# Performance work log

Measured on AMD Instinct MI355X. Metric: run time of the kernel, lower is better.

Reference implementation:

```python
import jax, jax.numpy as jnp
import numpy as np

N, MAX_NB, H, L, V, B, M = 16384, 15, 512, 128, 1024, 256, 65536


def setup_inputs() -> dict:
    key = jax.random.key(0)
    ks = jax.random.split(key, 32)
    s = 0.02  # param init scale
    inp = {
        'x_ids': jax.random.randint(ks[0], (N,), 0, V, dtype=jnp.int32),
        'contexts': jax.random.randint(ks[1], (N,), 0, B, dtype=jnp.int32),
        'nei_idx': jax.random.randint(ks[2], (N, MAX_NB), 0, M, dtype=jnp.int32),
        'nei_mask': jax.random.randint(ks[3], (N, MAX_NB), 0, 2, dtype=jnp.int32),
        'o_idx': jax.random.randint(ks[4], (N, MAX_NB), 0, M, dtype=jnp.int32),
        'o_mask': jax.random.randint(ks[5], (N, MAX_NB), 0, 2, dtype=jnp.int32),
        'H_msg': jax.random.normal(ks[6], (M, H), jnp.float32),
        'x_tree_vecs': jax.random.normal(ks[7], (B, L), jnp.float32),
        'embedding': jax.random.normal(ks[8], (V, H), jnp.float32) * s,
        'Wz_w': jax.random.normal(ks[9], (H, 2 * H), jnp.float32) * s,
        'Wz_b': jnp.zeros((H,), jnp.float32),
        'Wr_w': jax.random.normal(ks[10], (H, H), jnp.float32) * s,
        'Wr_b': jnp.zeros((H,), jnp.float32),
        'Ur_w': jax.random.normal(ks[11], (H, H), jnp.float32) * s,
        'Wh_w': jax.random.normal(ks[12], (H, 2 * H), jnp.float32) * s,
        'Wh_b': jnp.zeros((H,), jnp.float32),
        'W_w': jax.random.normal(ks[13], (H, H + L), jnp.float32) * s,
        'W_b': jnp.zeros((H,), jnp.float32),
        'Wo_w': jax.random.normal(ks[14], (V, H), jnp.float32) * s,
        'Wo_b': jnp.zeros((V,), jnp.float32),
        'Ui_w': jax.random.normal(ks[15], (H, 2 * H), jnp.float32) * s,
        'Ui_b': jnp.zeros((H,), jnp.float32),
        'U_w': jax.random.normal(ks[16], (H, H + L), jnp.float32) * s,
        'U_b': jnp.zeros((H,), jnp.float32),
        'Uo_w': jax.random.normal(ks[17], (1, H), jnp.float32) * s,
        'Uo_b': jnp.zeros((1,), jnp.float32),
    }
    return inp


def _gru(x, h_nei, Wz_w, Wz_b, Wr_w, Wr_b, Ur_w, Wh_w, Wh_b):
    # x: [N,H], h_nei: [N,MAX_NB,H]
    sum_h = h_nei.sum(axis=1)
    z = jax.nn.sigmoid(jnp.concatenate([x, sum_h], axis=1) @ Wz_w.T + Wz_b)
    r1 = (x @ Wr_w.T + Wr_b)[:, None, :]          # [N,1,H]
    r2 = jnp.einsum('nkh,gh->nkg', h_nei, Ur_w)   # U_r(h_nei), no bias
    r = jax.nn.sigmoid(r1 + r2)
    sum_gated = (r * h_nei).sum(axis=1)
    pre_h = jnp.tanh(jnp.concatenate([x, sum_gated], axis=1) @ Wh_w.T + Wh_b)
    return (1.0 - z) * sum_h + z * pre_h


def reference(x_ids, contexts, nei_idx, nei_mask, o_idx, o_mask, H_msg,
              x_tree_vecs, embedding, Wz_w, Wz_b, Wr_w, Wr_b, Ur_w,
              Wh_w, Wh_b, W_w, W_b, Wo_w, Wo_b, Ui_w, Ui_b, U_w, U_b,
              Uo_w, Uo_b):
    x = embedding[x_ids]                                   # [N,H]
    h_nei = H_msg[nei_idx] * nei_mask[..., None].astype(H_msg.dtype)  # [N,NB,H]
    o_nei = H_msg[o_idx] * o_mask[..., None].astype(H_msg.dtype)
    new_h = _gru(x, h_nei, Wz_w, Wz_b, Wr_w, Wr_b, Ur_w, Wh_w, Wh_b)
    cur_o = o_nei.sum(axis=1)                              # [N,H]
    ctx = x_tree_vecs[contexts]                            # [N,L]
    # word prediction: aggregate(new_h, contexts, x_tree_vecs, 'word')
    w_hid = jax.nn.relu(jnp.concatenate([new_h, ctx], axis=1) @ W_w.T + W_b)
    word_scores = w_hid @ Wo_w.T + Wo_b                    # [N,V]
    # stop prediction: U_i(cat(x, cur_o)) -> aggregate(..., 'stop')
    stop_h = jax.nn.relu(jnp.concatenate([x, cur_o], axis=1) @ Ui_w.T + Ui_b)
    s_hid = jax.nn.relu(jnp.concatenate([stop_h, ctx], axis=1) @ U_w.T + U_b)
    stop_scores = s_hid @ Uo_w.T + Uo_b                    # [N,1]
    return jnp.concatenate([word_scores, stop_scores], axis=1)  # [N,V+1]
```

## Files before the change

### kernel.cpp

```cpp
#include <hip/hip_runtime.h>
#include <hip/hip_bf16.h>

typedef unsigned short u16;
typedef unsigned int u32;
typedef __attribute__((ext_vector_type(8))) short s8v;
typedef __attribute__((ext_vector_type(4))) float f4v;

#define HDIM 512
#define NNODE 16384
#define NB 15

__device__ __forceinline__ u16 f2bu(float x) {
  union { float f; u32 i; } v; v.f = x;
  u32 r = v.i + 0x7FFFu + ((v.i >> 16) & 1u);
  return (u16)(r >> 16);
}
__device__ __forceinline__ float bu2f(u16 u) {
  union { u32 i; float f; } v; v.i = ((u32)u) << 16;
  return v.f;
}
__device__ __forceinline__ u32 pk(float a, float b) {
  return (u32)f2bu(a) | ((u32)f2bu(b) << 16);
}
__device__ __forceinline__ float sigm(float x) {
  return __builtin_amdgcn_rcpf(1.f + __expf(-x));
}
__device__ __forceinline__ void gl16(const void* g, void* l) {
  __builtin_amdgcn_global_load_lds(
      (const __attribute__((address_space(1))) u32*)g,
      (__attribute__((address_space(3))) u32*)l, 16, 0, 0);
}

__global__ __launch_bounds__(256) void k_cvt_all(
    const float* Wz_w, const float* Wr_w, const float* Wh_w, const float* Ui_w,
    const float* Ur_w, const float* W_w, const float* U_w, const float* Wo_w,
    const float* emb, const float* xtree,
    const float* Wz_b, const float* Wr_b, const float* Wh_b, const float* Ui_b,
    const float* W_b, const float* U_b,
    u16* wcat, u16* wz_h, u16* wh_h, u16* ui_h, u16* ur, u16* w_n, u16* u_n,
    u16* ccat, u16* wo, u16* emb_bf, u16* xt_bf, float* ebias, float* cbias) {
  int seg = blockIdx.y;
  const float* src = nullptr; u16* dst = nullptr;
  const float* fsrc = nullptr; float* fdst = nullptr;
  int R = 0, Cs = 0, c0 = 0, C = 0, fn = 0;
  switch (seg) {
    case 0:  src = Wz_w; dst = wcat;              R = 512;  Cs = 1024; c0 = 0;   C = 512; break;
    case 1:  src = Wr_w; dst = wcat + 512 * 512;  R = 512;  Cs = 512;  c0 = 0;   C = 512; break;
    case 2:  src = Wh_w; dst = wcat + 1024 * 512; R = 512;  Cs = 1024; c0 = 0;   C = 512; break;
    case 3:  src = Ui_w; dst = wcat + 1536 * 512; R = 512;  Cs = 1024; c0 = 0;   C = 512; break;
    case 4:  src = Wz_w; dst = wz_h;              R = 512;  Cs = 1024; c0 = 512; C = 512; break;
    case 5:  src = Wh_w; dst = wh_h;              R = 512;  Cs = 1024; c0 = 512; C = 512; break;
    case 6:  src = Ui_w; dst = ui_h;              R = 512;  Cs = 1024; c0 = 512; C = 512; break;
    case 7:  src = Ur_w; dst = ur;                R = 512;  Cs = 512;  c0 = 0;   C = 512; break;
    case 8:  src = W_w;  dst = w_n;               R = 512;  Cs = 640;  c0 = 0;   C = 512; break;
    case 9:  src = U_w;  dst = u_n;               R = 512;  Cs = 640;  c0 = 0;   C = 512; break;
    case 10: src = W_w;  dst = ccat;              R = 512;  Cs = 640;  c0 = 512; C = 128; break;
    case 11: src = U_w;  dst = ccat + 512 * 128;  R = 512;  Cs = 640;  c0 = 512; C = 128; break;
    case 12: src = Wo_w; dst = wo;                R = 1024; Cs = 512;  c0 = 0;   C = 512; break;
    case 13: src = emb;  dst = emb_bf;            R = 1024; Cs = 512;  c0 = 0;   C = 512; break;
    case 14: src = xtree; dst = xt_bf;            R = 256;  Cs = 128;  c0 = 0;   C = 128; break;
    case 15: fsrc = Wz_b; fdst = ebias;        fn = 512; break;
    case 16: fsrc = Wr_b; fdst = ebias + 512;  fn = 512; break;
    case 17: fsrc = Wh_b; fdst = ebias + 1024; fn = 512; break;
    case 18: fsrc = Ui_b; fdst = ebias + 1536; fn = 512; break;
    case 19: fsrc = W_b;  fdst = cbias;        fn = 512; break;
    case 20: fsrc = U_b;  fdst = cbias + 512;  fn = 512; break;
  }
  int i = blockIdx.x * 256 + threadIdx.x;
  if (fdst) { if (i < fn) fdst[i] = fsrc[i]; return; }
  int e0 = i * 8;
  if (e0 >= R * C) return;
  int r = e0 / C, c = e0 - r * C;
  const float* s = src + (size_t)r * Cs + c0 + c;
  float4 a = *reinterpret_cast<const float4*>(s);
  float4 b = *reinterpret_cast<const float4*>(s + 4);
  uint4 o = {pk(a.x, a.y), pk(a.z, a.w), pk(b.x, b.y), pk(b.z, b.w)};
  *reinterpret_cast<uint4*>(&dst[e0]) = o;
}

__global__ void k_cvtH(const float* __restrict__ src, u16* __restrict__ HR) {
  size_t i = ((size_t)blockIdx.x * 256 + threadIdx.x) * 8;
  size_t m = i >> 9, c = i & 511;
  float4 a = *reinterpret_cast<const float4*>(src + i);
  float4 b = *reinterpret_cast<const float4*>(src + i + 4);
  uint4 o = {pk(a.x, a.y), pk(a.z, a.w), pk(b.x, b.y), pk(b.z, b.w)};
  *reinterpret_cast<uint4*>(&HR[m * 1024 + c]) = o;
}

struct GP {
  const u16* A; const u16* B; int K; int lda;
  const float* gadd; int ldg; const int* gidx;
  const float* bias; const u16* shb;
  float* outf; u16* outh; int ldo;
};

template<int EP>
__device__ __forceinline__ void epi(int row, int col, float v, const GP& g) {
  if constexpr (EP == 0) {
    g.outf[(size_t)row * g.ldo + col] = v + (g.bias ? g.bias[col] : 0.f);
  } else if constexpr (EP == 3) {
    float pre = v + g.gadd[(size_t)g.gidx[row] * g.ldg + col];
    g.outh[(size_t)row * g.ldo + col] = f2bu(pre > 0.f ? pre : 0.f);
  } else {
    g.outh[(size_t)row * g.ldo + col] = f2bu(v);
  }
}

template<int EP>
__device__ void gemm_core(const GP& g, u16* AsB, u16* BsB) {
  const int tid = threadIdx.x, lane = tid & 63, w = tid >> 6;
  const int wm = (w >> 2) * 64, wn = (w & 3) * 32;
  const int nx = gridDim.x;
  int orig = blockIdx.y * nx + blockIdx.x;
  int q = (nx * gridDim.y) >> 3;
  int tile = (orig & 7) * q + (orig >> 3);
  const int n0 = (tile % nx) * 128, m0 = (tile / nx) * 128;
  const int K = g.K;

  const u16* gA[2]; const u16* gB[2]; int ls[2];
#pragma unroll
  for (int i = 0; i < 2; i++) {
    int slot = tid + i * 512;
    int r = slot >> 3, c = (slot & 7) ^ (r & 7);
    gA[i] = g.A + (size_t)(m0 + r) * g.lda + c * 8;
    gB[i] = g.B + (size_t)(n0 + r) * K + c * 8;
    ls[i] = slot * 8;
  }

  f4v acc[4][2];
  f4v z4 = {0.f, 0.f, 0.f, 0.f};
#pragma unroll
  for (int a = 0; a < 4; a++) { acc[a][0] = z4; acc[a][1] = z4; }

  const int T = K >> 6;
#pragma unroll
  for (int i = 0; i < 2; i++) gl16(gA[i], AsB + ls[i]);
#pragma unroll
  for (int i = 0; i < 2; i++) gl16(gB[i], BsB + ls[i]);

  int cur = 0;
  for (int t = 0; t < T; t++) {
    __syncthreads();
    if (t + 1 < T) {
      int k0 = (t + 1) * 64;
      u16* as = AsB + (cur ^ 1) * 8192;
      u16* bs = BsB + (cur ^ 1) * 8192;
#pragma unroll
      for (int i = 0; i < 2; i++) gl16(gA[i] + k0, as + ls[i]);
#pragma unroll
      for (int i = 0; i < 2; i++) gl16(gB[i] + k0, bs + ls[i]);
    }
    const u16* as = AsB + cur * 8192;
    const u16* bs = BsB + cur * 8192;
#pragma unroll
    for (int ks = 0; ks < 2; ks++) {
      s8v af[4], bf[2];
      int cc = ks * 4 + (lane >> 4);
#pragma unroll
      for (int i = 0; i < 4; i++) {
        int R = wm + i * 16 + (lane & 15);
        af[i] = *reinterpret_cast<const s8v*>(&as[R * 64 + (cc ^ (R & 7)) * 8]);
      }
#pragma unroll
      for (int i = 0; i < 2; i++) {
        int C = wn + i * 16 + (lane & 15);
        bf[i] = *reinterpret_cast<const s8v*>(&bs[C * 64 + (cc ^ (C & 7)) * 8]);
      }
#pragma unroll
      for (int mi = 0; mi < 4; mi++)
#pragma unroll
        for (int ni = 0; ni < 2; ni++)
          acc[mi][ni] = __builtin_amdgcn_mfma_f32_16x16x32_bf16(
              af[mi], bf[ni], acc[mi][ni], 0, 0, 0);
    }
    cur ^= 1;
  }
#pragma unroll
  for (int mi = 0; mi < 4; mi++)
#pragma unroll
    for (int ni = 0; ni < 2; ni++)
#pragma unroll
      for (int r = 0; r < 4; r++) {
        int row = m0 + wm + mi * 16 + (lane >> 4) * 4 + r;
        int col = n0 + wn + ni * 16 + (lane & 15);
        epi<EP>(row, col, acc[mi][ni][r], g);
      }
}

template<int EP>
__global__ __launch_bounds__(512, 4) void k_gemm(GP g) {
  __shared__ u16 As[2 * 128 * 64], Bs[2 * 128 * 64];
  gemm_core<EP>(g, As, Bs);
}

template<int EPa, int EPb>
__global__ __launch_bounds__(512, 4) void k_pair(GP a, GP b) {
  __shared__ u16 As[2 * 128 * 64], Bs[2 * 128 * 64];
  if (blockIdx.z == 0) gemm_core<EPa>(a, As, Bs);
  else gemm_core<EPb>(b, As, Bs);
}

__global__ __launch_bounds__(512, 4) void k_zn(
    const u16* __restrict__ sumh, const u16* __restrict__ sg,
    const u16* __restrict__ Wz, const u16* __restrict__ Wh,
    const float* __restrict__ E_z, const float* __restrict__ E_h, int ldg,
    const int* __restrict__ gidx, u16* __restrict__ newh) {
  __shared__ u16 As1[128 * 64], Bs1[128 * 64], As2[128 * 64], Bs2[128 * 64];
  const int tid = threadIdx.x, lane = tid & 63, w = tid >> 6;
  const int wm = (w >> 2) * 64, wn = (w & 3) * 32;
  const int nx = gridDim.x;
  int orig = blockIdx.y * nx + blockIdx.x;
  int q = (nx * gridDim.y) >> 3;
  int tile = (orig & 7) * q + (orig >> 3);
  const int n0 = (tile % nx) * 128, m0 = (tile / nx) * 128;

  const u16 *gA1[2], *gA2[2], *gB1[2], *gB2[2]; int ls[2];
#pragma unroll
  for (int i = 0; i < 2; i++) {
    int slot = tid + i * 512;
    int r = slot >> 3, c = (slot & 7) ^ (r & 7);
    gA1[i] = sumh + (size_t)(m0 + r) * HDIM + c * 8;
    gA2[i] = sg + (size_t)(m0 + r) * HDIM + c * 8;
    gB1[i] = Wz + (size_t)(n0 + r) * HDIM + c * 8;
    gB2[i] = Wh + (size_t)(n0 + r) * HDIM + c * 8;
    ls[i] = slot * 8;
  }

  f4v az[4][2], ah[4][2];
  f4v z4 = {0.f, 0.f, 0.f, 0.f};
#pragma unroll
  for (int a = 0; a < 4; a++) {
    az[a][0] = z4; az[a][1] = z4; ah[a][0] = z4; ah[a][1] = z4;
  }

  for (int k0 = 0; k0 < HDIM; k0 += 64) {
    __syncthreads();
#pragma unroll
    for (int i = 0; i < 2; i++) gl16(gA1[i] + k0, As1 + ls[i]);
#pragma unroll
    for (int i = 0; i < 2; i++) gl16(gB1[i] + k0, Bs1 + ls[i]);
#pragma unroll
    for (int i = 0; i < 2; i++) gl16(gA2[i] + k0, As2 + ls[i]);
#pragma unroll
    for (int i = 0; i < 2; i++) gl16(gB2[i] + k0, Bs2 + ls[i]);
    __syncthreads();
#pragma unroll
    for (int ks = 0; ks < 2; ks++) {
      int cc = ks * 4 + (lane >> 4);
      {
        s8v af[4], bf[2];
#pragma unroll
        for (int i = 0; i < 4; i++) {
          int R = wm + i * 16 + (lane & 15);
          af[i] = *reinterpret_cast<const s8v*>(&As1[R * 64 + (cc ^ (R & 7)) * 8]);
        }
#pragma unroll
        for (int i = 0; i < 2; i++) {
          int C = wn + i * 16 + (lane & 15);
          bf[i] = *reinterpret_cast<const s8v*>(&Bs1[C * 64 + (cc ^ (C & 7)) * 8]);
        }
#pragma unroll
        for (int mi = 0; mi < 4; mi++)
#pragma unroll
          for (int ni = 0; ni < 2; ni++)
            az[mi][ni] = __builtin_amdgcn_mfma_f32_16x16x32_bf16(
                af[mi], bf[ni], az[mi][ni], 0, 0, 0);
      }
      {
        s8v af[4], bf[2];
#pragma unroll
        for (int i = 0; i < 4; i++) {
          int R = wm + i * 16 + (lane & 15);
          af[i] = *reinterpret_cast<const s8v*>(&As2[R * 64 + (cc ^ (R & 7)) * 8]);
        }
#pragma unroll
        for (int i = 0; i < 2; i++) {
          int C = wn + i * 16 + (lane & 15);
          bf[i] = *reinterpret_cast<const s8v*>(&Bs2[C * 64 + (cc ^ (C & 7)) * 8]);
        }
#pragma unroll
        for (int mi = 0; mi < 4; mi++)
#pragma unroll
          for (int ni = 0; ni < 2; ni++)
            ah[mi][ni] = __builtin_amdgcn_mfma_f32_16x16x32_bf16(
                af[mi], bf[ni], ah[mi][ni], 0, 0, 0);
      }
    }
  }
#pragma unroll
  for (int mi = 0; mi < 4; mi++)
#pragma unroll
    for (int r = 0; r < 4; r++) {
      int row = m0 + wm + mi * 16 + (lane >> 4) * 4 + r;
      int xid = gidx[row];
      const float* ez = E_z + (size_t)xid * ldg;
      const float* eh = E_h + (size_t)xid * ldg;
#pragma unroll
      for (int ni = 0; ni < 2; ni++) {
        int col = n0 + wn + ni * 16 + (lane & 15);
        float zv = sigm(az[mi][ni][r] + ez[col]);
        float pre = tanhf(ah[mi][ni][r] + eh[col]);
        float sh = bu2f(sumh[(size_t)row * HDIM + col]);
        newh[(size_t)row * HDIM + col] = f2bu((1.f - zv) * sh + zv * pre);
      }
    }
}

__global__ __launch_bounds__(256) void k_gsr(
    const u16* __restrict__ HR,
    const float* __restrict__ E_r, int ldg, const int* __restrict__ x_ids,
    const int* __restrict__ nei_idx, const int* __restrict__ nei_mask,
    const int* __restrict__ o_idx, const int* __restrict__ o_mask,
    u16* __restrict__ sum_h_bf, u16* __restrict__ sg_bf,
    u16* __restrict__ cur_o_bf) {
  int n = blockIdx.x;
  int t = threadIdx.x;
  __shared__ int sidx[NB], smsk[NB], soid[NB], somk[NB];
  __shared__ int sx;
  if (t < NB) {
    sidx[t] = nei_idx[(size_t)n * NB + t];
    smsk[t] = nei_mask[(size_t)n * NB + t];
  } else if (t >= 64 && t < 64 + NB) {
    int k = t - 64;
    soid[k] = o_idx[(size_t)n * NB + k];
    somk[k] = o_mask[(size_t)n * NB + k];
  } else if (t == 128) {
    sx = x_ids[n];
  }
  __syncthreads();
  int c = t * 2;
  const float2 e = *reinterpret_cast<const float2*>(E_r + (size_t)sx * ldg + c);
  float s0 = 0.f, s1 = 0.f, g0 = 0.f, g1 = 0.f, o0 = 0.f, o1 = 0.f;
#pragma unroll
  for (int k = 0; k < NB; k++) {
    if (smsk[k]) {
      const u16* row = HR + (size_t)sidx[k] * 1024;
      u32 hv = *reinterpret_cast<const u32*>(row + c);
      u32 rv = *reinterpret_cast<const u32*>(row + 512 + c);
      float h0 = bu2f((u16)hv), h1 = bu2f((u16)(hv >> 16));
      float r0 = sigm(bu2f((u16)rv) + e.x);
      float r1 = sigm(bu2f((u16)(rv >> 16)) + e.y);
      s0 += h0; s1 += h1;
      g0 += r0 * h0; g1 += r1 * h1;
    }
    if (somk[k]) {
      u32 v = *reinterpret_cast<const u32*>(HR + (size_t)soid[k] * 1024 + c);
      o0 += bu2f((u16)v); o1 += bu2f((u16)(v >> 16));
    }
  }
  size_t b = (size_t)n * HDIM + c;
  *reinterpret_cast<u32*>(&sum_h_bf[b]) = pk(s0, s1);
  *reinterpret_cast<u32*>(&sg_bf[b]) = pk(g0, g1);
  *reinterpret_cast<u32*>(&cur_o_bf[b]) = pk(o0, o1);
}

__global__ __launch_bounds__(256) void k_stop(
    const u16* __restrict__ shid, const float* __restrict__ Uo_w,
    const float* __restrict__ Uo_b, float* __restrict__ out) {
  int n = blockIdx.x * 4 + (threadIdx.x >> 6);
  int lane = threadIdx.x & 63;
  float s = 0.f;
  for (int j = lane; j < HDIM; j += 64)
    s += bu2f(shid[(size_t)n * HDIM + j]) * Uo_w[j];
#pragma unroll
  for (int off = 32; off; off >>= 1) s += __shfl_xor(s, off, 64);
  if (lane == 0) out[(size_t)n * 1025 + 1024] = s + Uo_b[0];
}

extern "C" void kernel_launch(void* const* d_in, const int* in_sizes, int n_in,
                              void* d_out, int out_size, void* d_ws, size_t ws_size,
                              hipStream_t stream) {
  const int* x_ids = (const int*)d_in[0];
  const int* contexts = (const int*)d_in[1];
  const int* nei_idx = (const int*)d_in[2];
  const int* nei_mask = (const int*)d_in[3];
  const int* o_idx = (const int*)d_in[4];
  const int* o_mask = (const int*)d_in[5];
  const float* H_msg = (const float*)d_in[6];
  const float* xtree = (const float*)d_in[7];
  const float* emb = (const float*)d_in[8];
  const float* Wz_w = (const float*)d_in[9];  const float* Wz_b = (const float*)d_in[10];
  const float* Wr_w = (const float*)d_in[11]; const float* Wr_b = (const float*)d_in[12];
  const float* Ur_w = (const float*)d_in[13];
  const float* Wh_w = (const float*)d_in[14]; const float* Wh_b = (const float*)d_in[15];
  const float* W_w  = (const float*)d_in[16]; const float* W_b  = (const float*)d_in[17];
  const float* Wo_w = (const float*)d_in[18]; const float* Wo_b = (const float*)d_in[19];
  const float* Ui_w = (const float*)d_in[20]; const float* Ui_b = (const float*)d_in[21];
  const float* U_w  = (const float*)d_in[22]; const float* U_b  = (const float*)d_in[23];
  const float* Uo_w = (const float*)d_in[24]; const float* Uo_b = (const float*)d_in[25];
  float* out = (float*)d_out;
  const int M = 65536;

  char* base = (char*)d_ws;
  size_t ofs = 0;
  auto alloc = [&](size_t bytes) -> char* {
    char* p = base + ofs;
    ofs = (ofs + bytes + 255) & ~(size_t)255;
    return p;
  };
  u16* wcat  = (u16*)alloc((size_t)2048 * 512 * 2);
  u16* wz_h  = (u16*)alloc(512 * 512 * 2);
  u16* wh_h  = (u16*)alloc(512 * 512 * 2);
  u16* ui_h  = (u16*)alloc(512 * 512 * 2);
  u16* ur    = (u16*)alloc(512 * 512 * 2);
  u16* w_n   = (u16*)alloc(512 * 512 * 2);
  u16* u_n   = (u16*)alloc(512 * 512 * 2);
  u16* ccat  = (u16*)alloc(1024 * 128 * 2);
  u16* wo    = (u16*)alloc(1024 * 512 * 2);
  u16* emb_bf = (u16*)alloc(1024 * 512 * 2);
  u16* xt_bf  = (u16*)alloc(256 * 128 * 2);
  float* ebias = (float*)alloc(2048 * 4);
  float* cbias = (float*)alloc(1024 * 4);
  float* E_cat = (float*)alloc((size_t)1024 * 2048 * 4);
  float* C_cat = (float*)alloc((size_t)256 * 1024 * 4);
  u16* HR = (u16*)alloc((size_t)M * 1024 * 2);
  u16* sum_h_bf = (u16*)alloc((size_t)NNODE * HDIM * 2);
  u16* cur_o_bf = (u16*)alloc((size_t)NNODE * HDIM * 2);
  u16* sg_bf    = (u16*)alloc((size_t)NNODE * HDIM * 2);
  u16* newh_bf  = (u16*)alloc((size_t)NNODE * HDIM * 2);
  u16* whid_bf  = (u16*)alloc((size_t)NNODE * HDIM * 2);
  u16* stoph_bf = (u16*)alloc((size_t)NNODE * HDIM * 2);
  u16* shid_bf  = (u16*)alloc((size_t)NNODE * HDIM * 2);

  k_cvt_all<<<dim3(256, 21), dim3(256), 0, stream>>>(
      Wz_w, Wr_w, Wh_w, Ui_w, Ur_w, W_w, U_w, Wo_w, emb, xtree,
      Wz_b, Wr_b, Wh_b, Ui_b, W_b, U_b,
      wcat, wz_h, wh_h, ui_h, ur, w_n, u_n, ccat, wo, emb_bf, xt_bf,
      ebias, cbias);
  k_cvtH<<<dim3(16384), dim3(256), 0, stream>>>(H_msg, HR);

  GP ge{emb_bf, wcat, 512, 512, nullptr, 0, nullptr, ebias, nullptr,
        E_cat, nullptr, 2048};
  k_gemm<0><<<dim3(16, 8), dim3(512), 0, stream>>>(ge);
  GP gc{xt_bf, ccat, 128, 128, nullptr, 0, nullptr, cbias, nullptr,
        C_cat, nullptr, 1024};
  k_gemm<0><<<dim3(8, 2), dim3(512), 0, stream>>>(gc);

  GP gr{HR, ur, 512, 1024, nullptr, 0, nullptr, nullptr, nullptr,
        nullptr, HR + 512, 1024};
  k_gemm<4><<<dim3(4, 512), dim3(512), 0, stream>>>(gr);

  k_gsr<<<dim3(NNODE), dim3(256), 0, stream>>>(
      HR, E_cat + 512, 2048, x_ids, nei_idx, nei_mask, o_idx, o_mask,
      sum_h_bf, sg_bf, cur_o_bf);

  GP gs{cur_o_bf, ui_h, 512, 512, E_cat + 1536, 2048, x_ids, nullptr, nullptr,
        nullptr, stoph_bf, 512};
  k_gemm<3><<<dim3(4, 128), dim3(512), 0, stream>>>(gs);

  k_zn<<<dim3(4, 128), dim3(512), 0, stream>>>(
      sum_h_bf, sg_bf, wz_h, wh_h, E_cat, E_cat + 1024, 2048, x_ids, newh_bf);

  GP gw{newh_bf, w_n, 512, 512, C_cat, 1024, contexts, nullptr, nullptr,
        nullptr, whid_bf, 512};
  GP gu{stoph_bf, u_n, 512, 512, C_cat + 512, 1024, contexts, nullptr, nullptr,
        nullptr, shid_bf, 512};
  k_pair<3, 3><<<dim3(4, 128, 2), dim3(512), 0, stream>>>(gw, gu);

  GP gword{whid_bf, wo, 512, 512, nullptr, 0, nullptr, Wo_b, nullptr,
           out, nullptr, 1025};
  k_gemm<0><<<dim3(8, 128), dim3(512), 0, stream>>>(gword);

  k_stop<<<dim3(NNODE / 4), dim3(256), 0, stream>>>(shid_bf, Uo_w, Uo_b, out);
}
```

Baseline: 333.0 us.

## Use 4-stage K=32 pipelined GEMM with vmcnt waits; widen gather kernel per thread

The shared GEMM core goes from a double-buffered K=64 tile with a __syncthreads per step to a 4-deep ring of K=32 tiles. It issues loads three stages ahead and waits with explicit s_waitcnt vmcnt plus a raw s_barrier, with K made a compile-time template parameter so the loop fully unrolls. Separately, the gather/sum kernel now handles two nodes per block and four columns per thread with 8-byte loads and stores. The aim is to hide global-to-LDS latency better and cut barrier and instruction overhead. The cost is less MFMA work per barrier, and correctness now depends on exact vmcnt accounting.

```diff
diff --git a/kernel.cpp b/kernel.cpp
--- a/kernel.cpp
+++ b/kernel.cpp
@@ -29,6 +29,11 @@
   __builtin_amdgcn_global_load_lds(
       (const __attribute__((address_space(1))) u32*)g,
       (__attribute__((address_space(3))) u32*)l, 16, 0, 0);
+}
+template<int N> __device__ __forceinline__ void wait_vm() {
+  if constexpr (N == 0) asm volatile("s_waitcnt vmcnt(0)" ::: "memory");
+  else if constexpr (N == 2) asm volatile("s_waitcnt vmcnt(2)" ::: "memory");
+  else asm volatile("s_waitcnt vmcnt(4)" ::: "memory");
 }
 
 __global__ __launch_bounds__(256) void k_cvt_all(
@@ -106,7 +111,7 @@
   }
 }
 
-template<int EP>
+template<int EP, int KV>
 __device__ void gemm_core(const GP& g, u16* AsB, u16* BsB) {
   const int tid = threadIdx.x, lane = tid & 63, w = tid >> 6;
   const int wm = (w >> 2) * 64, wn = (w & 3) * 32;
@@ -115,65 +120,53 @@
   int q = (nx * gridDim.y) >> 3;
   int tile = (orig & 7) * q + (orig >> 3);
   const int n0 = (tile % nx) * 128, m0 = (tile / nx) * 128;
-  const int K = g.K;
-
-  const u16* gA[2]; const u16* gB[2]; int ls[2];
-#pragma unroll
-  for (int i = 0; i < 2; i++) {
-    int slot = tid + i * 512;
-    int r = slot >> 3, c = (slot & 7) ^ (r & 7);
-    gA[i] = g.A + (size_t)(m0 + r) * g.lda + c * 8;
-    gB[i] = g.B + (size_t)(n0 + r) * K + c * 8;
-    ls[i] = slot * 8;
-  }
+
+  const int sr = tid >> 2, sc = (tid & 3) ^ (sr & 3);
+  const u16* gA = g.A + (size_t)(m0 + sr) * g.lda + sc * 8;
+  const u16* gB = g.B + (size_t)(n0 + sr) * KV + sc * 8;
+  const int ls = tid * 8;
 
   f4v acc[4][2];
   f4v z4 = {0.f, 0.f, 0.f, 0.f};
 #pragma unroll
   for (int a = 0; a < 4; a++) { acc[a][0] = z4; acc[a][1] = z4; }
 
-  const int T = K >> 6;
-#pragma unroll
-  for (int i = 0; i < 2; i++) gl16(gA[i], AsB + ls[i]);
-#pragma unroll
-  for (int i = 0; i < 2; i++) gl16(gB[i], BsB + ls[i]);
-
-  int cur = 0;
+  constexpr int T = KV / 32;
+  auto STAGE = [&](int t) {
+    int buf = (t & 3) * 4096;
+    gl16(gA + t * 32, AsB + buf + ls);
+    gl16(gB + t * 32, BsB + buf + ls);
+  };
+  STAGE(0); STAGE(1); STAGE(2);
+
+#pragma unroll
   for (int t = 0; t < T; t++) {
-    __syncthreads();
-    if (t + 1 < T) {
-      int k0 = (t + 1) * 64;
-      u16* as = AsB + (cur ^ 1) * 8192;
-      u16* bs = BsB + (cur ^ 1) * 8192;
-#pragma unroll
-      for (int i = 0; i < 2; i++) gl16(gA[i] + k0, as + ls[i]);
-#pragma unroll
-      for (int i = 0; i < 2; i++) gl16(gB[i] + k0, bs + ls[i]);
-    }
-    const u16* as = AsB + cur * 8192;
-    const u16* bs = BsB + cur * 8192;
-#pragma unroll
-    for (int ks = 0; ks < 2; ks++) {
-      s8v af[4], bf[2];
-      int cc = ks * 4 + (lane >> 4);
-#pragma unroll
-      for (int i = 0; i < 4; i++) {
-        int R = wm + i * 16 + (lane & 15);
-        af[i] = *reinterpret_cast<const s8v*>(&as[R * 64 + (cc ^ (R & 7)) * 8]);
-      }
-#pragma unroll
-      for (int i = 0; i < 2; i++) {
-        int C = wn + i * 16 + (lane & 15);
-        bf[i] = *reinterpret_cast<const s8v*>(&bs[C * 64 + (cc ^ (C & 7)) * 8]);
-      }
-#pragma unroll
-      for (int mi = 0; mi < 4; mi++)
-#pragma unroll
-        for (int ni = 0; ni < 2; ni++)
-          acc[mi][ni] = __builtin_amdgcn_mfma_f32_16x16x32_bf16(
-              af[mi], bf[ni], acc[mi][ni], 0, 0, 0);
-    }
-    cur ^= 1;
+    if (t < T - 2) wait_vm<4>();
+    else if (t == T - 2) wait_vm<2>();
+    else wait_vm<0>();
+    __builtin_amdgcn_s_barrier();
+    asm volatile("" ::: "memory");
+    if (t + 3 < T) STAGE(t + 3);
+    const u16* as = AsB + (t & 3) * 4096;
+    const u16* bs = BsB + (t & 3) * 4096;
+    s8v af[4], bf[2];
+    int cc = lane >> 4;
+#pragma unroll
+    for (int i = 0; i < 4; i++) {
+      int R = wm + i * 16 + (lane & 15);
+      af[i] = *reinterpret_cast<const s8v*>(&as[R * 32 + (cc ^ (R & 3)) * 8]);
+    }
+#pragma unroll
+    for (int i = 0; i < 2; i++) {
+      int C = wn + i * 16 + (lane & 15);
+      bf[i] = *reinterpret_cast<const s8v*>(&bs[C * 32 + (cc ^ (C & 3)) * 8]);
+    }
+#pragma unroll
+    for (int mi = 0; mi < 4; mi++)
+#pragma unroll
+      for (int ni = 0; ni < 2; ni++)
+        acc[mi][ni] = __builtin_amdgcn_mfma_f32_16x16x32_bf16(
+            af[mi], bf[ni], acc[mi][ni], 0, 0, 0);
   }
 #pragma unroll
   for (int mi = 0; mi < 4; mi++)
@@ -187,17 +180,17 @@
       }
 }
 
-template<int EP>
+template<int EP, int KV>
 __global__ __launch_bounds__(512, 4) void k_gemm(GP g) {
-  __shared__ u16 As[2 * 128 * 64], Bs[2 * 128 * 64];
-  gemm_core<EP>(g, As, Bs);
-}
-
-template<int EPa, int EPb>
+  __shared__ u16 As[4 * 4096], Bs[4 * 4096];
+  gemm_core<EP, KV>(g, As, Bs);
+}
+
+template<int EPa, int EPb, int KV>
 __global__ __launch_bounds__(512, 4) void k_pair(GP a, GP b) {
-  __shared__ u16 As[2 * 128 * 64], Bs[2 * 128 * 64];
-  if (blockIdx.z == 0) gemm_core<EPa>(a, As, Bs);
-  else gemm_core<EPb>(b, As, Bs);
+  __shared__ u16 As[4 * 4096], Bs[4 * 4096];
+  if (blockIdx.z == 0) gemm_core<EPa, KV>(a, As, Bs);
+  else gemm_core<EPb, KV>(b, As, Bs);
 }
 
 __global__ __launch_bounds__(512, 4) void k_zn(
@@ -313,45 +306,54 @@
     const int* __restrict__ o_idx, const int* __restrict__ o_mask,
     u16* __restrict__ sum_h_bf, u16* __restrict__ sg_bf,
     u16* __restrict__ cur_o_bf) {
-  int n = blockIdx.x;
   int t = threadIdx.x;
-  __shared__ int sidx[NB], smsk[NB], soid[NB], somk[NB];
-  __shared__ int sx;
-  if (t < NB) {
-    sidx[t] = nei_idx[(size_t)n * NB + t];
-    smsk[t] = nei_mask[(size_t)n * NB + t];
-  } else if (t >= 64 && t < 64 + NB) {
-    int k = t - 64;
-    soid[k] = o_idx[(size_t)n * NB + k];
-    somk[k] = o_mask[(size_t)n * NB + k];
-  } else if (t == 128) {
-    sx = x_ids[n];
+  int nd = t >> 7, lt = t & 127;
+  int n = blockIdx.x * 2 + nd;
+  __shared__ int sidx[2][NB], smsk[2][NB], soid[2][NB], somk[2][NB];
+  __shared__ int sx[2];
+  if (lt < NB) {
+    sidx[nd][lt] = nei_idx[(size_t)n * NB + lt];
+    smsk[nd][lt] = nei_mask[(size_t)n * NB + lt];
+  } else if (lt >= 32 && lt < 32 + NB) {
+    int k = lt - 32;
+    soid[nd][k] = o_idx[(size_t)n * NB + k];
+    somk[nd][k] = o_mask[(size_t)n * NB + k];
+  } else if (lt == 64) {
+    sx[nd] = x_ids[n];
   }
   __syncthreads();
-  int c = t * 2;
-  const float2 e = *reinterpret_cast<const float2*>(E_r + (size_t)sx * ldg + c);
-  float s0 = 0.f, s1 = 0.f, g0 = 0.f, g1 = 0.f, o0 = 0.f, o1 = 0.f;
+  int c = lt * 4;
+  float4 e = *reinterpret_cast<const float4*>(E_r + (size_t)sx[nd] * ldg + c);
+  float s0 = 0.f, s1 = 0.f, s2 = 0.f, s3 = 0.f;
+  float g0 = 0.f, g1 = 0.f, g2 = 0.f, g3 = 0.f;
+  float o0 = 0.f, o1 = 0.f, o2 = 0.f, o3 = 0.f;
 #pragma unroll
   for (int k = 0; k < NB; k++) {
-    if (smsk[k]) {
-      const u16* row = HR + (size_t)sidx[k] * 1024;
-      u32 hv = *reinterpret_cast<const u32*>(row + c);
-      u32 rv = *reinterpret_cast<const u32*>(row + 512 + c);
-      float h0 = bu2f((u16)hv), h1 = bu2f((u16)(hv >> 16));
-      float r0 = sigm(bu2f((u16)rv) + e.x);
-      float r1 = sigm(bu2f((u16)(rv >> 16)) + e.y);
-      s0 += h0; s1 += h1;
-      g0 += r0 * h0; g1 += r1 * h1;
-    }
-    if (somk[k]) {
-      u32 v = *reinterpret_cast<const u32*>(HR + (size_t)soid[k] * 1024 + c);
-      o0 += bu2f((u16)v); o1 += bu2f((u16)(v >> 16));
+    if (smsk[nd][k]) {
+      const u16* row = HR + (size_t)sidx[nd][k] * 1024;
+      uint2 hv = *reinterpret_cast<const uint2*>(row + c);
+      uint2 rv = *reinterpret_cast<const uint2*>(row + 512 + c);
+      float h0 = bu2f((u16)hv.x), h1 = bu2f((u16)(hv.x >> 16));
+      float h2 = bu2f((u16)hv.y), h3 = bu2f((u16)(hv.y >> 16));
+      s0 += h0; s1 += h1; s2 += h2; s3 += h3;
+      g0 += sigm(bu2f((u16)rv.x) + e.x) * h0;
+      g1 += sigm(bu2f((u16)(rv.x >> 16)) + e.y) * h1;
+      g2 += sigm(bu2f((u16)rv.y) + e.z) * h2;
+      g3 += sigm(bu2f((u16)(rv.y >> 16)) + e.w) * h3;
+    }
+    if (somk[nd][k]) {
+      uint2 ov = *reinterpret_cast<const uint2*>(HR + (size_t)soid[nd][k] * 1024 + c);
+      o0 += bu2f((u16)ov.x); o1 += bu2f((u16)(ov.x >> 16));
+      o2 += bu2f((u16)ov.y); o3 += bu2f((u16)(ov.y >> 16));
     }
   }
   size_t b = (size_t)n * HDIM + c;
-  *reinterpret_cast<u32*>(&sum_h_bf[b]) = pk(s0, s1);
-  *reinterpret_cast<u32*>(&sg_bf[b]) = pk(g0, g1);
-  *reinterpret_cast<u32*>(&cur_o_bf[b]) = pk(o0, o1);
+  uint2 ps = {pk(s0, s1), pk(s2, s3)};
+  uint2 pg = {pk(g0, g1), pk(g2, g3)};
+  uint2 po = {pk(o0, o1), pk(o2, o3)};
+  *reinterpret_cast<uint2*>(&sum_h_bf[b]) = ps;
+  *reinterpret_cast<uint2*>(&sg_bf[b]) = pg;
+  *reinterpret_cast<uint2*>(&cur_o_bf[b]) = po;
 }
 
 __global__ __launch_bounds__(256) void k_stop(
@@ -431,22 +433,22 @@
 
   GP ge{emb_bf, wcat, 512, 512, nullptr, 0, nullptr, ebias, nullptr,
         E_cat, nullptr, 2048};
-  k_gemm<0><<<dim3(16, 8), dim3(512), 0, stream>>>(ge);
+  k_gemm<0, 512><<<dim3(16, 8), dim3(512), 0, stream>>>(ge);
   GP gc{xt_bf, ccat, 128, 128, nullptr, 0, nullptr, cbias, nullptr,
         C_cat, nullptr, 1024};
-  k_gemm<0><<<dim3(8, 2), dim3(512), 0, stream>>>(gc);
+  k_gemm<0, 128><<<dim3(8, 2), dim3(512), 0, stream>>>(gc);
 
   GP gr{HR, ur, 512, 1024, nullptr, 0, nullptr, nullptr, nullptr,
         nullptr, HR + 512, 1024};
-  k_gemm<4><<<dim3(4, 512), dim3(512), 0, stream>>>(gr);
-
-  k_gsr<<<dim3(NNODE), dim3(256), 0, stream>>>(
+  k_gemm<4, 512><<<dim3(4, 512), dim3(512), 0, stream>>>(gr);
+
+  k_gsr<<<dim3(NNODE / 2), dim3(256), 0, stream>>>(
       HR, E_cat + 512, 2048, x_ids, nei_idx, nei_mask, o_idx, o_mask,
       sum_h_bf, sg_bf, cur_o_bf);
 
   GP gs{cur_o_bf, ui_h, 512, 512, E_cat + 1536, 2048, x_ids, nullptr, nullptr,
         nullptr, stoph_bf, 512};
-  k_gemm<3><<<dim3(4, 128), dim3(512), 0, stream>>>(gs);
+  k_gemm<3, 512><<<dim3(4, 128), dim3(512), 0, stream>>>(gs);
 
   k_zn<<<dim3(4, 128), dim3(512), 0, stream>>>(
       sum_h_bf, sg_bf, wz_h, wh_h, E_cat, E_cat + 1024, 2048, x_ids, newh_bf);
@@ -455,11 +457,11 @@
         nullptr, whid_bf, 512};
   GP gu{stoph_bf, u_n, 512, 512, C_cat + 512, 1024, contexts, nullptr, nullptr,
         nullptr, shid_bf, 512};
-  k_pair<3, 3><<<dim3(4, 128, 2), dim3(512), 0, stream>>>(gw, gu);
+  k_pair<3, 3, 512><<<dim3(4, 128, 2), dim3(512), 0, stream>>>(gw, gu);
 
   GP gword{whid_bf, wo, 512, 512, nullptr, 0, nullptr, Wo_b, nullptr,
            out, nullptr, 1025};
-  k_gemm<0><<<dim3(8, 128), dim3(512), 0, stream>>>(gword);
+  k_gemm<0, 512><<<dim3(8, 128), dim3(512), 0, stream>>>(gword);
 
   k_stop<<<dim3(NNODE / 4), dim3(256), 0, stream>>>(shid_bf, Uo_w, Uo_b, out);
 }
```

Result: no change. 331.8 us (-0.4%).
